# Kernel optimization log

Measured on AMD Instinct MI355X. Metric: run time of the kernel, lower is better.

Reference implementation:

```python
import jax, jax.numpy as jnp
import numpy as np

HIDDEN = 100
N_NODE = 100000
B = 512
T = 50

def setup_inputs() -> dict:
    key = jax.random.key(0)
    ks = jax.random.split(key, 20)
    stdv = 1.0 / np.sqrt(HIDDEN)
    u = lambda k, shape: jax.random.uniform(k, shape, jnp.float32, -stdv, stdv)
    d = HIDDEN
    return {
        "adj_in": jax.random.uniform(ks[0], (B, T, T), jnp.float32),
        "adj_out": jax.random.uniform(ks[1], (B, T, T), jnp.float32),
        "mask": jnp.ones((B, T), jnp.float32),
        "item": jax.random.randint(ks[2], (B, T), 0, N_NODE, jnp.int32),
        "alias": jax.random.randint(ks[3], (B, T), 0, T, jnp.int32),
        "step": 1,
        "embedding": u(ks[4], (N_NODE, d)),
        "W_in": u(ks[5], (d, d)),
        "b_in": u(ks[6], (d,)),
        "W_out": u(ks[7], (d, d)),
        "b_out": u(ks[8], (d,)),
        "gru_gate_k": u(ks[9], (3 * d, 2 * d)),
        "gru_gate_b": jnp.ones((2 * d,), jnp.float32),  # TF GRUCell gate bias init = 1.0
        "gru_cand_k": u(ks[10], (3 * d, d)),
        "gru_cand_b": jnp.zeros((d,), jnp.float32),
        "nasr_w1": u(ks[11], (d, d)),
        "nasr_w2": u(ks[12], (d, d)),
        "nasr_v": u(ks[13], (1, d)),
        "nasr_b": jnp.zeros((d,), jnp.float32),
        "B_mat": u(ks[14], (2 * d, d)),
    }


def _ggnn(item, adj_in, adj_out, embedding, W_in, b_in, W_out, b_out,
          gru_gate_k, gru_gate_b, gru_cand_k, gru_cand_b, step):
    h = embedding[item]  # [B,T,d]
    d = h.shape[-1]
    for _ in range(step):
        a_in = jnp.einsum('bts,bsd->btd', adj_in, h @ W_in + b_in)
        a_out = jnp.einsum('bts,bsd->btd', adj_out, h @ W_out + b_out)
        a = jnp.concatenate([a_in, a_out], axis=-1)  # [B,T,2d]
        # TF GRUCell: gates then candidate
        gates = jax.nn.sigmoid(jnp.concatenate([a, h], -1) @ gru_gate_k + gru_gate_b)
        r, u_ = gates[..., :d], gates[..., d:]
        c = jnp.tanh(jnp.concatenate([a, r * h], -1) @ gru_cand_k + gru_cand_b)
        h = u_ * h + (1.0 - u_) * c
    return h  # [B,T,d]


def reference(adj_in, adj_out, mask, item, alias, step, embedding,
              W_in, b_in, W_out, b_out, gru_gate_k, gru_gate_b,
              gru_cand_k, gru_cand_b, nasr_w1, nasr_w2, nasr_v, nasr_b, B_mat):
    d = embedding.shape[1]
    re_emb = _ggnn(item, adj_in, adj_out, embedding, W_in, b_in, W_out, b_out,
                   gru_gate_k, gru_gate_b, gru_cand_k, gru_cand_b, step)
    rm = jnp.sum(jax.lax.stop_gradient(mask), axis=1)  # session lengths
    bidx = jnp.arange(re_emb.shape[0])
    last_id = alias[bidx, rm.astype(jnp.int32) - 1]          # [B]
    last_h = re_emb[bidx, last_id]                            # [B,d]
    seq_h = jnp.take_along_axis(re_emb, alias[..., None], axis=1)  # [B,L,d]
    last = last_h @ nasr_w1                                   # [B,d]
    seq = seq_h @ nasr_w2                                     # [B,L,d]
    m = jax.nn.sigmoid(last[:, None, :] + seq + nasr_b)       # [B,L,d]
    coef = (m @ nasr_v[0]) * mask                             # [B,L]
    ma = jnp.concatenate([jnp.sum(coef[..., None] * seq_h, axis=1), last], axis=-1)  # [B,2d]
    y1 = ma @ B_mat                                           # [B,d]
    logits = y1 @ embedding[1:].T                             # [B,n_node-1]
    return logits
```

## Files before the change

### kernel.cpp

```cpp
#include <hip/hip_runtime.h>
#include <math.h>

#define D 100
#define T 50
#define BB 512
#define NOUT 99999

__device__ __forceinline__ float sigf(float x) { return 1.f / (1.f + expf(-x)); }

__global__ __launch_bounds__(256) void ggnn_fused(
    const float* __restrict__ adj_in, const float* __restrict__ adj_out,
    const float* __restrict__ mask,   const int* __restrict__ item,
    const int* __restrict__ alias_,   const float* __restrict__ emb,
    const float* __restrict__ W_in,   const float* __restrict__ b_in,
    const float* __restrict__ W_out,  const float* __restrict__ b_out,
    const float* __restrict__ gate_k, const float* __restrict__ gate_b,
    const float* __restrict__ cand_k, const float* __restrict__ cand_b,
    const float* __restrict__ w1,     const float* __restrict__ w2,
    const float* __restrict__ v,      const float* __restrict__ nb,
    const float* __restrict__ Bm,     float* __restrict__ y1)
{
    __shared__ float hS[T*D];
    __shared__ float R1[T*D];
    __shared__ float R2[T*D];
    __shared__ float maskS[T+2], vS[D], nbS[D], lastWS[D], coefS[T+2], maS[2*D];
    __shared__ int aliasS[T+2];
    __shared__ int rmidx;

    const int b = blockIdx.x, tid = threadIdx.x;
    const size_t bT = (size_t)b * T;

    if (tid < T) {
        aliasS[tid] = alias_[bT + tid];
        maskS[tid]  = mask[bT + tid];
    }
    if (tid >= 64 && tid < 64 + D) {
        int k = tid - 64;
        vS[k] = v[k]; nbS[k] = nb[k];
    }
    for (int idx = tid; idx < T*25; idx += 256) {
        int t = idx / 25, q = idx - t*25;
        int node = item[bT + t];
        *(float4*)&hS[t*D + q*4] = *(const float4*)&emb[(size_t)node*D + q*4];
    }
    __syncthreads();
    if (tid == 0) {
        float s = 0.f;
        for (int t = 0; t < T; ++t) s += maskS[t];
        rmidx = aliasS[(int)s - 1];
    }

    const bool act250 = tid < 250;
    const int tg50  = tid / 50;
    const int rem50 = tid % 50;
    const int cg25  = tid / 25;
    const int jq25  = tid % 25;

    if (act250) {
        const int which = rem50 / 25, jq = rem50 % 25;
        const int t0 = tg50 * 10;
        const float* W  = which ? W_out : W_in;
        const float* bb = which ? b_out : b_in;
        float4 binit = *(const float4*)&bb[jq*4];
        float4 acc[10];
        #pragma unroll
        for (int tt = 0; tt < 10; ++tt) acc[tt] = binit;
        for (int k = 0; k < D; k += 2) {
            float4 wa = *(const float4*)&W[k*D + jq*4];
            float4 wb = *(const float4*)&W[(k+1)*D + jq*4];
            #pragma unroll
            for (int tt = 0; tt < 10; ++tt) {
                float2 a = *(const float2*)&hS[(t0+tt)*D + k];
                acc[tt].x += a.x*wa.x + a.y*wb.x;
                acc[tt].y += a.x*wa.y + a.y*wb.y;
                acc[tt].z += a.x*wa.z + a.y*wb.z;
                acc[tt].w += a.x*wa.w + a.y*wb.w;
            }
        }
        float* dst = which ? R2 : R1;
        #pragma unroll
        for (int tt = 0; tt < 10; ++tt)
            *(float4*)&dst[(t0+tt)*D + jq*4] = acc[tt];
    }
    __syncthreads();

    float4 eacc[10];
    if (act250) {
        const int which = rem50 / 25, jq = rem50 % 25;
        const int t0 = tg50 * 10;
        const float* adj = which ? adj_out : adj_in;
        const float* Xs  = which ? R2 : R1;
        #pragma unroll
        for (int tt = 0; tt < 10; ++tt) eacc[tt] = make_float4(0.f,0.f,0.f,0.f);
        #pragma unroll 2
        for (int s = 0; s < T; ++s) {
            float4 x = *(const float4*)&Xs[s*D + jq*4];
            const float* ap = &adj[(bT + t0)*T + s];
            #pragma unroll
            for (int tt = 0; tt < 10; ++tt) {
                float a = ap[tt*T];
                eacc[tt].x += a*x.x; eacc[tt].y += a*x.y;
                eacc[tt].z += a*x.z; eacc[tt].w += a*x.w;
            }
        }
    }
    __syncthreads();
    if (act250) {
        const int which = rem50 / 25, jq = rem50 % 25;
        const int t0 = tg50 * 10;
        float* dst = which ? R2 : R1;
        #pragma unroll
        for (int tt = 0; tt < 10; ++tt)
            *(float4*)&dst[(t0+tt)*D + jq*4] = eacc[tt];
    }
    __syncthreads();

    float4 gacc[10];
    if (act250) {
        const int nq = rem50;
        const int t0 = tg50 * 10;
        float4 ginit = *(const float4*)&gate_b[nq*4];
        #pragma unroll
        for (int tt = 0; tt < 10; ++tt) gacc[tt] = ginit;
        for (int k = 0; k < D; k += 2) {
            float4 g0a = *(const float4*)&gate_k[(size_t)k*200 + nq*4];
            float4 g0b = *(const float4*)&gate_k[(size_t)(k+1)*200 + nq*4];
            float4 g1a = *(const float4*)&gate_k[(size_t)(k+100)*200 + nq*4];
            float4 g1b = *(const float4*)&gate_k[(size_t)(k+101)*200 + nq*4];
            float4 g2a = *(const float4*)&gate_k[(size_t)(k+200)*200 + nq*4];
            float4 g2b = *(const float4*)&gate_k[(size_t)(k+201)*200 + nq*4];
            #pragma unroll
            for (int tt = 0; tt < 10; ++tt) {
                float2 a0 = *(const float2*)&R1[(t0+tt)*D + k];
                float2 a1 = *(const float2*)&R2[(t0+tt)*D + k];
                float2 a2 = *(const float2*)&hS[(t0+tt)*D + k];
                gacc[tt].x += a0.x*g0a.x + a0.y*g0b.x + a1.x*g1a.x + a1.y*g1b.x + a2.x*g2a.x + a2.y*g2b.x;
                gacc[tt].y += a0.x*g0a.y + a0.y*g0b.y + a1.x*g1a.y + a1.y*g1b.y + a2.x*g2a.y + a2.y*g2b.y;
                gacc[tt].z += a0.x*g0a.z + a0.y*g0b.z + a1.x*g1a.z + a1.y*g1b.z + a2.x*g2a.z + a2.y*g2b.z;
                gacc[tt].w += a0.x*g0a.w + a0.y*g0b.w + a1.x*g1a.w + a1.y*g1b.w + a2.x*g2a.w + a2.y*g2b.w;
            }
        }
        #pragma unroll
        for (int tt = 0; tt < 10; ++tt) {
            gacc[tt].x = sigf(gacc[tt].x); gacc[tt].y = sigf(gacc[tt].y);
            gacc[tt].z = sigf(gacc[tt].z); gacc[tt].w = sigf(gacc[tt].w);
        }
    }

    float4 cacc[5];
    if (act250) {
        const int t0 = cg25 * 5;
        float4 cinit = *(const float4*)&cand_b[jq25*4];
        #pragma unroll
        for (int tt = 0; tt < 5; ++tt) cacc[tt] = cinit;
        for (int k = 0; k < D; k += 2) {
            float4 c0a = *(const float4*)&cand_k[(size_t)k*D + jq25*4];
            float4 c0b = *(const float4*)&cand_k[(size_t)(k+1)*D + jq25*4];
            float4 c1a = *(const float4*)&cand_k[(size_t)(k+100)*D + jq25*4];
            float4 c1b = *(const float4*)&cand_k[(size_t)(k+101)*D + jq25*4];
            #pragma unroll
            for (int tt = 0; tt < 5; ++tt) {
                float2 a0 = *(const float2*)&R1[(t0+tt)*D + k];
                float2 a1 = *(const float2*)&R2[(t0+tt)*D + k];
                cacc[tt].x += a0.x*c0a.x + a0.y*c0b.x + a1.x*c1a.x + a1.y*c1b.x;
                cacc[tt].y += a0.x*c0a.y + a0.y*c0b.y + a1.x*c1a.y + a1.y*c1b.y;
                cacc[tt].z += a0.x*c0a.z + a0.y*c0b.z + a1.x*c1a.z + a1.y*c1b.z;
                cacc[tt].w += a0.x*c0a.w + a0.y*c0b.w + a1.x*c1a.w + a1.y*c1b.w;
            }
        }
    }
    __syncthreads();

    if (act250) {
        const int nq = rem50;
        const int t0 = tg50 * 10;
        if (nq < 25) {
            #pragma unroll
            for (int tt = 0; tt < 10; ++tt) {
                float4 hh = *(const float4*)&hS[(t0+tt)*D + nq*4];
                float4 g = gacc[tt];
                float4 o; o.x = g.x*hh.x; o.y = g.y*hh.y; o.z = g.z*hh.z; o.w = g.w*hh.w;
                *(float4*)&R1[(t0+tt)*D + nq*4] = o;
            }
        } else {
            #pragma unroll
            for (int tt = 0; tt < 10; ++tt)
                *(float4*)&R2[(t0+tt)*D + (nq-25)*4] = gacc[tt];
        }
    }
    __syncthreads();

    if (act250) {
        const int t0 = cg25 * 5;
        for (int k = 0; k < D; k += 2) {
            float4 c2a = *(const float4*)&cand_k[(size_t)(k+200)*D + jq25*4];
            float4 c2b = *(const float4*)&cand_k[(size_t)(k+201)*D + jq25*4];
            #pragma unroll
            for (int tt = 0; tt < 5; ++tt) {
                float2 rh = *(const float2*)&R1[(t0+tt)*D + k];
                cacc[tt].x += rh.x*c2a.x + rh.y*c2b.x;
                cacc[tt].y += rh.x*c2a.y + rh.y*c2b.y;
                cacc[tt].z += rh.x*c2a.z + rh.y*c2b.z;
                cacc[tt].w += rh.x*c2a.w + rh.y*c2b.w;
            }
        }
        #pragma unroll
        for (int tt = 0; tt < 5; ++tt) {
            float4 c4;
            c4.x = tanhf(cacc[tt].x); c4.y = tanhf(cacc[tt].y);
            c4.z = tanhf(cacc[tt].z); c4.w = tanhf(cacc[tt].w);
            float4 u4 = *(const float4*)&R2[(t0+tt)*D + jq25*4];
            float4 hh = *(const float4*)&hS[(t0+tt)*D + jq25*4];
            float4 o;
            o.x = u4.x*hh.x + (1.f-u4.x)*c4.x;
            o.y = u4.y*hh.y + (1.f-u4.y)*c4.y;
            o.z = u4.z*hh.z + (1.f-u4.z)*c4.z;
            o.w = u4.w*hh.w + (1.f-u4.w)*c4.w;
            *(float4*)&hS[(t0+tt)*D + jq25*4] = o;
        }
    }
    __syncthreads();

    if (tid < 125) {
        const int sg = tid / 25, jq = tid % 25;
        const int t0 = sg * 10;
        float4 sacc[10];
        #pragma unroll
        for (int tt = 0; tt < 10; ++tt) sacc[tt] = make_float4(0.f,0.f,0.f,0.f);
        int at[10];
        #pragma unroll
        for (int tt = 0; tt < 10; ++tt) at[tt] = aliasS[t0+tt];
        for (int k = 0; k < D; k += 2) {
            float4 wa = *(const float4*)&w2[(size_t)k*D + jq*4];
            float4 wb = *(const float4*)&w2[(size_t)(k+1)*D + jq*4];
            #pragma unroll
            for (int tt = 0; tt < 10; ++tt) {
                float2 a = *(const float2*)&hS[at[tt]*D + k];
                sacc[tt].x += a.x*wa.x + a.y*wb.x;
                sacc[tt].y += a.x*wa.y + a.y*wb.y;
                sacc[tt].z += a.x*wa.z + a.y*wb.z;
                sacc[tt].w += a.x*wa.w + a.y*wb.w;
            }
        }
        #pragma unroll
        for (int tt = 0; tt < 10; ++tt)
            *(float4*)&R1[(t0+tt)*D + jq*4] = sacc[tt];
    } else if (tid >= 128 && tid < 153) {
        const int jq = tid - 128;
        const int lid = rmidx;
        float4 acc = make_float4(0.f,0.f,0.f,0.f);
        for (int k = 0; k < D; k += 2) {
            float4 wa = *(const float4*)&w1[(size_t)k*D + jq*4];
            float4 wb = *(const float4*)&w1[(size_t)(k+1)*D + jq*4];
            float2 a = *(const float2*)&hS[lid*D + k];
            acc.x += a.x*wa.x + a.y*wb.x;
            acc.y += a.x*wa.y + a.y*wb.y;
            acc.z += a.x*wa.z + a.y*wb.z;
            acc.w += a.x*wa.w + a.y*wb.w;
        }
        *(float4*)&lastWS[jq*4] = acc;
    }
    __syncthreads();

    if (tid < T) {
        float s = 0.f;
        #pragma unroll 4
        for (int k = 0; k < D; ++k) {
            float x = lastWS[k] + R1[tid*D + k] + nbS[k];
            s += vS[k] * sigf(x);
        }
        coefS[tid] = s * maskS[tid];
    }
    __syncthreads();
    if (tid < 25) {
        float4 acc = make_float4(0.f,0.f,0.f,0.f);
        #pragma unroll 5
        for (int t = 0; t < T; ++t) {
            float c = coefS[t];
            float4 hh = *(const float4*)&hS[aliasS[t]*D + tid*4];
            acc.x += c*hh.x; acc.y += c*hh.y; acc.z += c*hh.z; acc.w += c*hh.w;
        }
        *(float4*)&maS[tid*4] = acc;
    } else if (tid >= 32 && tid < 57) {
        int j4 = tid - 32;
        *(float4*)&maS[D + j4*4] = *(const float4*)&lastWS[j4*4];
    }
    __syncthreads();
    if (tid < 25) {
        float4 acc = make_float4(0.f,0.f,0.f,0.f);
        #pragma unroll 4
        for (int k = 0; k < 2*D; ++k) {
            float a = maS[k];
            float4 w = *(const float4*)&Bm[(size_t)k*D + tid*4];
            acc.x += a*w.x; acc.y += a*w.y; acc.z += a*w.z; acc.w += a*w.w;
        }
        *(float4*)&y1[(size_t)b*D + tid*4] = acc;
    }
}

#define LDB 132

#define GB_COMPUTE(Ab, kbase) do {                                            \
    _Pragma("unroll")                                                         \
    for (int kk = 0; kk < 4; ++kk) {                                          \
        float4 b0 = *(const float4*)&Bs[(kbase + kk)*LDB + tx*4];             \
        float4 b1 = *(const float4*)&Bs[(kbase + kk)*LDB + 64 + tx*4];        \
        _Pragma("unroll")                                                     \
        for (int i = 0; i < 8; ++i) {                                         \
            float a_ = kk==0 ? Ab[i].x : kk==1 ? Ab[i].y :                    \
                       kk==2 ? Ab[i].z : Ab[i].w;                             \
            acc[i][0] += a_*b0.x; acc[i][1] += a_*b0.y;                       \
            acc[i][2] += a_*b0.z; acc[i][3] += a_*b0.w;                       \
            acc[i][4] += a_*b1.x; acc[i][5] += a_*b1.y;                       \
            acc[i][6] += a_*b1.z; acc[i][7] += a_*b1.w;                       \
        }                                                                     \
    }                                                                         \
} while (0)

__global__ __launch_bounds__(256) void gemm_big(
    const float* __restrict__ y1,
    const float* __restrict__ emb,
    float* __restrict__ out)
{
    __shared__ float Bs[100*LDB];
    const int tid = threadIdx.x;
    const int tx = tid & 15, ty = tid >> 4;
    const int n0 = blockIdx.x * 128;

    for (int idx = tid; idx < 128*25; idx += 256) {
        int n = idx / 25, q = idx - n*25;
        int gn = n0 + n;
        float4 vv = make_float4(0.f,0.f,0.f,0.f);
        if (gn < NOUT) vv = *(const float4*)&emb[(size_t)(gn+1)*D + q*4];
        int w = n & 63;
        int pos = (n & 64) + ((w & 15) << 2) + (w >> 4);
        Bs[(q*4+0)*LDB + pos] = vv.x;
        Bs[(q*4+1)*LDB + pos] = vv.y;
        Bs[(q*4+2)*LDB + pos] = vv.z;
        Bs[(q*4+3)*LDB + pos] = vv.w;
    }
    __syncthreads();

    float acc[8][8];
    float4 A0[8], A1[8];

    #pragma unroll 1
    for (int mc = 0; mc < 2; ++mc) {
        const int m0 = blockIdx.y * 256 + mc * 128;

        #pragma unroll
        for (int i = 0; i < 8; ++i)
            #pragma unroll
            for (int j = 0; j < 8; ++j) acc[i][j] = 0.f;

        #pragma unroll
        for (int i = 0; i < 8; ++i)
            A0[i] = *(const float4*)&y1[(size_t)(m0 + ty + i*16)*D + 0];

        int k = 0;
        #pragma unroll 1
        for (int it = 0; it < 12; ++it, k += 8) {
            #pragma unroll
            for (int i = 0; i < 8; ++i)
                A1[i] = *(const float4*)&y1[(size_t)(m0 + ty + i*16)*D + k + 4];
            GB_COMPUTE(A0, k);
            #pragma unroll
            for (int i = 0; i < 8; ++i)
                A0[i] = *(const float4*)&y1[(size_t)(m0 + ty + i*16)*D + k + 8];
            GB_COMPUTE(A1, k + 4);
        }
        GB_COMPUTE(A0, 96);

        #pragma unroll
        for (int i = 0; i < 8; ++i) {
            size_t row = (size_t)(m0 + ty + i*16) * NOUT;
            #pragma unroll
            for (int h = 0; h < 2; ++h)
                #pragma unroll
                for (int q = 0; q < 4; ++q) {
                    int n = n0 + h*64 + q*16 + tx;
                    if (n < NOUT) out[row + n] = acc[i][h*4+q];
                }
        }
    }
}

extern "C" void kernel_launch(void* const* d_in, const int* in_sizes, int n_in,
                              void* d_out, int out_size, void* d_ws, size_t ws_size,
                              hipStream_t stream)
{
    const float* adj_in  = (const float*)d_in[0];
    const float* adj_out = (const float*)d_in[1];
    const float* mask    = (const float*)d_in[2];
    const int*   item    = (const int*)  d_in[3];
    const int*   alias_  = (const int*)  d_in[4];
    const float* emb     = (const float*)d_in[6];
    const float* W_in    = (const float*)d_in[7];
    const float* b_in    = (const float*)d_in[8];
    const float* W_out   = (const float*)d_in[9];
    const float* b_out   = (const float*)d_in[10];
    const float* gate_k  = (const float*)d_in[11];
    const float* gate_b  = (const float*)d_in[12];
    const float* cand_k  = (const float*)d_in[13];
    const float* cand_b  = (const float*)d_in[14];
    const float* w1      = (const float*)d_in[15];
    const float* w2      = (const float*)d_in[16];
    const float* v       = (const float*)d_in[17];
    const float* nb      = (const float*)d_in[18];
    const float* Bm      = (const float*)d_in[19];
    float* out = (float*)d_out;
    float* y1  = (float*)d_ws;

    ggnn_fused<<<BB, 256, 0, stream>>>(
        adj_in, adj_out, mask, item, alias_, emb,
        W_in, b_in, W_out, b_out, gate_k, gate_b, cand_k, cand_b,
        w1, w2, v, nb, Bm, y1);

    gemm_big<<<dim3((NOUT + 127)/128, 2), 256, 0, stream>>>(y1, emb, out);
}
```

Before: 635.5 us.

## Double GGNN block to 512 threads with split-K shuffle reductions

The fused GGNN kernel now launches 512 threads per block instead of 256. Each thread handles 5 timesteps instead of 10, and the candidate and w2 projections are split across thread pairs along K, then combined with __shfl_xor. This aims to raise parallelism and latency hiding in the per-session kernel and to cut per-thread register pressure. The cost is extra shuffles and more idle threads in the serial tail phases, and the big logits GEMM, which likely dominates the runtime, is unchanged.

After: 629.6 us. No clear change (-0.9%).

```diff
diff --git a/kernel.cpp b/kernel.cpp
--- a/kernel.cpp
+++ b/kernel.cpp
@@ -8,7 +8,7 @@
 
 __device__ __forceinline__ float sigf(float x) { return 1.f / (1.f + expf(-x)); }
 
-__global__ __launch_bounds__(256) void ggnn_fused(
+__global__ __launch_bounds__(512, 4) void ggnn_fused(
     const float* __restrict__ adj_in, const float* __restrict__ adj_out,
     const float* __restrict__ mask,   const int* __restrict__ item,
     const int* __restrict__ alias_,   const float* __restrict__ emb,
@@ -38,7 +38,7 @@
         int k = tid - 64;
         vS[k] = v[k]; nbS[k] = nb[k];
     }
-    for (int idx = tid; idx < T*25; idx += 256) {
+    for (int idx = tid; idx < T*25; idx += 512) {
         int t = idx / 25, q = idx - t*25;
         int node = item[bT + t];
         *(float4*)&hS[t*D + q*4] = *(const float4*)&emb[(size_t)node*D + q*4];
@@ -50,26 +50,22 @@
         rmidx = aliasS[(int)s - 1];
     }
 
-    const bool act250 = tid < 250;
-    const int tg50  = tid / 50;
-    const int rem50 = tid % 50;
-    const int cg25  = tid / 25;
-    const int jq25  = tid % 25;
-
-    if (act250) {
-        const int which = rem50 / 25, jq = rem50 % 25;
-        const int t0 = tg50 * 10;
+    const bool act500 = tid < 500;
+
+    if (act500) {
+        const int which = tid / 250, rem = tid % 250;
+        const int jq = rem % 25, t0 = (rem / 25) * 5;
         const float* W  = which ? W_out : W_in;
         const float* bb = which ? b_out : b_in;
         float4 binit = *(const float4*)&bb[jq*4];
-        float4 acc[10];
-        #pragma unroll
-        for (int tt = 0; tt < 10; ++tt) acc[tt] = binit;
+        float4 acc[5];
+        #pragma unroll
+        for (int tt = 0; tt < 5; ++tt) acc[tt] = binit;
         for (int k = 0; k < D; k += 2) {
             float4 wa = *(const float4*)&W[k*D + jq*4];
             float4 wb = *(const float4*)&W[(k+1)*D + jq*4];
             #pragma unroll
-            for (int tt = 0; tt < 10; ++tt) {
+            for (int tt = 0; tt < 5; ++tt) {
                 float2 a = *(const float2*)&hS[(t0+tt)*D + k];
                 acc[tt].x += a.x*wa.x + a.y*wb.x;
                 acc[tt].y += a.x*wa.y + a.y*wb.y;
@@ -79,25 +75,25 @@
         }
         float* dst = which ? R2 : R1;
         #pragma unroll
-        for (int tt = 0; tt < 10; ++tt)
+        for (int tt = 0; tt < 5; ++tt)
             *(float4*)&dst[(t0+tt)*D + jq*4] = acc[tt];
     }
     __syncthreads();
 
-    float4 eacc[10];
-    if (act250) {
-        const int which = rem50 / 25, jq = rem50 % 25;
-        const int t0 = tg50 * 10;
+    float4 eacc[5];
+    if (act500) {
+        const int which = tid / 250, rem = tid % 250;
+        const int jq = rem % 25, t0 = (rem / 25) * 5;
         const float* adj = which ? adj_out : adj_in;
         const float* Xs  = which ? R2 : R1;
         #pragma unroll
-        for (int tt = 0; tt < 10; ++tt) eacc[tt] = make_float4(0.f,0.f,0.f,0.f);
+        for (int tt = 0; tt < 5; ++tt) eacc[tt] = make_float4(0.f,0.f,0.f,0.f);
         #pragma unroll 2
         for (int s = 0; s < T; ++s) {
             float4 x = *(const float4*)&Xs[s*D + jq*4];
             const float* ap = &adj[(bT + t0)*T + s];
             #pragma unroll
-            for (int tt = 0; tt < 10; ++tt) {
+            for (int tt = 0; tt < 5; ++tt) {
                 float a = ap[tt*T];
                 eacc[tt].x += a*x.x; eacc[tt].y += a*x.y;
                 eacc[tt].z += a*x.z; eacc[tt].w += a*x.w;
@@ -105,23 +101,23 @@
         }
     }
     __syncthreads();
-    if (act250) {
-        const int which = rem50 / 25, jq = rem50 % 25;
-        const int t0 = tg50 * 10;
+    if (act500) {
+        const int which = tid / 250, rem = tid % 250;
+        const int jq = rem % 25, t0 = (rem / 25) * 5;
         float* dst = which ? R2 : R1;
         #pragma unroll
-        for (int tt = 0; tt < 10; ++tt)
+        for (int tt = 0; tt < 5; ++tt)
             *(float4*)&dst[(t0+tt)*D + jq*4] = eacc[tt];
     }
     __syncthreads();
 
-    float4 gacc[10];
-    if (act250) {
-        const int nq = rem50;
-        const int t0 = tg50 * 10;
+    float4 gacc[5];
+    if (act500) {
+        const int nq = tid % 50;
+        const int t0 = (tid / 50) * 5;
         float4 ginit = *(const float4*)&gate_b[nq*4];
         #pragma unroll
-        for (int tt = 0; tt < 10; ++tt) gacc[tt] = ginit;
+        for (int tt = 0; tt < 5; ++tt) gacc[tt] = ginit;
         for (int k = 0; k < D; k += 2) {
             float4 g0a = *(const float4*)&gate_k[(size_t)k*200 + nq*4];
             float4 g0b = *(const float4*)&gate_k[(size_t)(k+1)*200 + nq*4];
@@ -130,7 +126,7 @@
             float4 g2a = *(const float4*)&gate_k[(size_t)(k+200)*200 + nq*4];
             float4 g2b = *(const float4*)&gate_k[(size_t)(k+201)*200 + nq*4];
             #pragma unroll
-            for (int tt = 0; tt < 10; ++tt) {
+            for (int tt = 0; tt < 5; ++tt) {
                 float2 a0 = *(const float2*)&R1[(t0+tt)*D + k];
                 float2 a1 = *(const float2*)&R2[(t0+tt)*D + k];
                 float2 a2 = *(const float2*)&hS[(t0+tt)*D + k];
@@ -141,42 +137,44 @@
             }
         }
         #pragma unroll
-        for (int tt = 0; tt < 10; ++tt) {
+        for (int tt = 0; tt < 5; ++tt) {
             gacc[tt].x = sigf(gacc[tt].x); gacc[tt].y = sigf(gacc[tt].y);
             gacc[tt].z = sigf(gacc[tt].z); gacc[tt].w = sigf(gacc[tt].w);
         }
     }
 
     float4 cacc[5];
-    if (act250) {
-        const int t0 = cg25 * 5;
-        float4 cinit = *(const float4*)&cand_b[jq25*4];
+    if (act500) {
+        const int jq = (tid >> 1) % 25;
+        const int t0 = ((tid >> 1) / 25) * 5;
+        const int kh = tid & 1;
+        const float* Ck = cand_k + (size_t)(kh ? 100 : 0) * D;
+        const float* As = kh ? R2 : R1;
+        float4 bq = *(const float4*)&cand_b[jq*4];
+        float4 cinit = kh ? make_float4(0.f,0.f,0.f,0.f) : bq;
         #pragma unroll
         for (int tt = 0; tt < 5; ++tt) cacc[tt] = cinit;
-        for (int k = 0; k < D; k += 2) {
-            float4 c0a = *(const float4*)&cand_k[(size_t)k*D + jq25*4];
-            float4 c0b = *(const float4*)&cand_k[(size_t)(k+1)*D + jq25*4];
-            float4 c1a = *(const float4*)&cand_k[(size_t)(k+100)*D + jq25*4];
-            float4 c1b = *(const float4*)&cand_k[(size_t)(k+101)*D + jq25*4];
-            #pragma unroll
-            for (int tt = 0; tt < 5; ++tt) {
-                float2 a0 = *(const float2*)&R1[(t0+tt)*D + k];
-                float2 a1 = *(const float2*)&R2[(t0+tt)*D + k];
-                cacc[tt].x += a0.x*c0a.x + a0.y*c0b.x + a1.x*c1a.x + a1.y*c1b.x;
-                cacc[tt].y += a0.x*c0a.y + a0.y*c0b.y + a1.x*c1a.y + a1.y*c1b.y;
-                cacc[tt].z += a0.x*c0a.z + a0.y*c0b.z + a1.x*c1a.z + a1.y*c1b.z;
-                cacc[tt].w += a0.x*c0a.w + a0.y*c0b.w + a1.x*c1a.w + a1.y*c1b.w;
-            }
-        }
-    }
-    __syncthreads();
-
-    if (act250) {
-        const int nq = rem50;
-        const int t0 = tg50 * 10;
+        for (int k = 0; k < 100; k += 2) {
+            float4 ca = *(const float4*)&Ck[(size_t)k*D + jq*4];
+            float4 cb = *(const float4*)&Ck[(size_t)(k+1)*D + jq*4];
+            #pragma unroll
+            for (int tt = 0; tt < 5; ++tt) {
+                float2 a = *(const float2*)&As[(t0+tt)*D + k];
+                cacc[tt].x += a.x*ca.x + a.y*cb.x;
+                cacc[tt].y += a.x*ca.y + a.y*cb.y;
+                cacc[tt].z += a.x*ca.z + a.y*cb.z;
+                cacc[tt].w += a.x*ca.w + a.y*cb.w;
+            }
+        }
+    }
+    __syncthreads();
+
+    if (act500) {
+        const int nq = tid % 50;
+        const int t0 = (tid / 50) * 5;
         if (nq < 25) {
             #pragma unroll
-            for (int tt = 0; tt < 10; ++tt) {
+            for (int tt = 0; tt < 5; ++tt) {
                 float4 hh = *(const float4*)&hS[(t0+tt)*D + nq*4];
                 float4 g = gacc[tt];
                 float4 o; o.x = g.x*hh.x; o.y = g.y*hh.y; o.z = g.z*hh.z; o.w = g.w*hh.w;
@@ -184,58 +182,72 @@
             }
         } else {
             #pragma unroll
-            for (int tt = 0; tt < 10; ++tt)
+            for (int tt = 0; tt < 5; ++tt)
                 *(float4*)&R2[(t0+tt)*D + (nq-25)*4] = gacc[tt];
         }
     }
     __syncthreads();
 
-    if (act250) {
-        const int t0 = cg25 * 5;
-        for (int k = 0; k < D; k += 2) {
-            float4 c2a = *(const float4*)&cand_k[(size_t)(k+200)*D + jq25*4];
-            float4 c2b = *(const float4*)&cand_k[(size_t)(k+201)*D + jq25*4];
-            #pragma unroll
-            for (int tt = 0; tt < 5; ++tt) {
-                float2 rh = *(const float2*)&R1[(t0+tt)*D + k];
-                cacc[tt].x += rh.x*c2a.x + rh.y*c2b.x;
-                cacc[tt].y += rh.x*c2a.y + rh.y*c2b.y;
-                cacc[tt].z += rh.x*c2a.z + rh.y*c2b.z;
-                cacc[tt].w += rh.x*c2a.w + rh.y*c2b.w;
+    if (act500) {
+        const int jq = (tid >> 1) % 25;
+        const int t0 = ((tid >> 1) / 25) * 5;
+        const int kh = tid & 1;
+        const float* Ck3 = cand_k + (size_t)(200 + kh*50) * D;
+        for (int k = 0; k < 50; k += 2) {
+            float4 ca = *(const float4*)&Ck3[(size_t)k*D + jq*4];
+            float4 cb = *(const float4*)&Ck3[(size_t)(k+1)*D + jq*4];
+            #pragma unroll
+            for (int tt = 0; tt < 5; ++tt) {
+                float2 rh = *(const float2*)&R1[(t0+tt)*D + kh*50 + k];
+                cacc[tt].x += rh.x*ca.x + rh.y*cb.x;
+                cacc[tt].y += rh.x*ca.y + rh.y*cb.y;
+                cacc[tt].z += rh.x*ca.z + rh.y*cb.z;
+                cacc[tt].w += rh.x*ca.w + rh.y*cb.w;
             }
         }
         #pragma unroll
         for (int tt = 0; tt < 5; ++tt) {
-            float4 c4;
-            c4.x = tanhf(cacc[tt].x); c4.y = tanhf(cacc[tt].y);
-            c4.z = tanhf(cacc[tt].z); c4.w = tanhf(cacc[tt].w);
-            float4 u4 = *(const float4*)&R2[(t0+tt)*D + jq25*4];
-            float4 hh = *(const float4*)&hS[(t0+tt)*D + jq25*4];
-            float4 o;
-            o.x = u4.x*hh.x + (1.f-u4.x)*c4.x;
-            o.y = u4.y*hh.y + (1.f-u4.y)*c4.y;
-            o.z = u4.z*hh.z + (1.f-u4.z)*c4.z;
-            o.w = u4.w*hh.w + (1.f-u4.w)*c4.w;
-            *(float4*)&hS[(t0+tt)*D + jq25*4] = o;
-        }
-    }
-    __syncthreads();
-
-    if (tid < 125) {
-        const int sg = tid / 25, jq = tid % 25;
-        const int t0 = sg * 10;
-        float4 sacc[10];
-        #pragma unroll
-        for (int tt = 0; tt < 10; ++tt) sacc[tt] = make_float4(0.f,0.f,0.f,0.f);
-        int at[10];
-        #pragma unroll
-        for (int tt = 0; tt < 10; ++tt) at[tt] = aliasS[t0+tt];
-        for (int k = 0; k < D; k += 2) {
-            float4 wa = *(const float4*)&w2[(size_t)k*D + jq*4];
-            float4 wb = *(const float4*)&w2[(size_t)(k+1)*D + jq*4];
-            #pragma unroll
-            for (int tt = 0; tt < 10; ++tt) {
-                float2 a = *(const float2*)&hS[at[tt]*D + k];
+            cacc[tt].x += __shfl_xor(cacc[tt].x, 1);
+            cacc[tt].y += __shfl_xor(cacc[tt].y, 1);
+            cacc[tt].z += __shfl_xor(cacc[tt].z, 1);
+            cacc[tt].w += __shfl_xor(cacc[tt].w, 1);
+        }
+        if (!kh) {
+            #pragma unroll
+            for (int tt = 0; tt < 5; ++tt) {
+                float4 c4;
+                c4.x = tanhf(cacc[tt].x); c4.y = tanhf(cacc[tt].y);
+                c4.z = tanhf(cacc[tt].z); c4.w = tanhf(cacc[tt].w);
+                float4 u4 = *(const float4*)&R2[(t0+tt)*D + jq*4];
+                float4 hh = *(const float4*)&hS[(t0+tt)*D + jq*4];
+                float4 o;
+                o.x = u4.x*hh.x + (1.f-u4.x)*c4.x;
+                o.y = u4.y*hh.y + (1.f-u4.y)*c4.y;
+                o.z = u4.z*hh.z + (1.f-u4.z)*c4.z;
+                o.w = u4.w*hh.w + (1.f-u4.w)*c4.w;
+                *(float4*)&hS[(t0+tt)*D + jq*4] = o;
+            }
+        }
+    }
+    __syncthreads();
+
+    if (act500) {
+        const int jq = (tid >> 1) % 25;
+        const int t0 = ((tid >> 1) / 25) * 5;
+        const int kh = tid & 1;
+        float4 sacc[5];
+        #pragma unroll
+        for (int tt = 0; tt < 5; ++tt) sacc[tt] = make_float4(0.f,0.f,0.f,0.f);
+        int at[5];
+        #pragma unroll
+        for (int tt = 0; tt < 5; ++tt) at[tt] = aliasS[t0+tt];
+        const float* Wp = w2 + (size_t)(kh*50) * D;
+        for (int k = 0; k < 50; k += 2) {
+            float4 wa = *(const float4*)&Wp[(size_t)k*D + jq*4];
+            float4 wb = *(const float4*)&Wp[(size_t)(k+1)*D + jq*4];
+            #pragma unroll
+            for (int tt = 0; tt < 5; ++tt) {
+                float2 a = *(const float2*)&hS[at[tt]*D + kh*50 + k];
                 sacc[tt].x += a.x*wa.x + a.y*wb.x;
                 sacc[tt].y += a.x*wa.y + a.y*wb.y;
                 sacc[tt].z += a.x*wa.z + a.y*wb.z;
@@ -243,22 +255,33 @@
             }
         }
         #pragma unroll
-        for (int tt = 0; tt < 10; ++tt)
-            *(float4*)&R1[(t0+tt)*D + jq*4] = sacc[tt];
-    } else if (tid >= 128 && tid < 153) {
-        const int jq = tid - 128;
+        for (int tt = 0; tt < 5; ++tt) {
+            sacc[tt].x += __shfl_xor(sacc[tt].x, 1);
+            sacc[tt].y += __shfl_xor(sacc[tt].y, 1);
+            sacc[tt].z += __shfl_xor(sacc[tt].z, 1);
+            sacc[tt].w += __shfl_xor(sacc[tt].w, 1);
+        }
+        if (!kh) {
+            #pragma unroll
+            for (int tt = 0; tt < 5; ++tt)
+                *(float4*)&R1[(t0+tt)*D + jq*4] = sacc[tt];
+        }
+    } else {
+        const int u = tid - 500;
         const int lid = rmidx;
-        float4 acc = make_float4(0.f,0.f,0.f,0.f);
-        for (int k = 0; k < D; k += 2) {
-            float4 wa = *(const float4*)&w1[(size_t)k*D + jq*4];
-            float4 wb = *(const float4*)&w1[(size_t)(k+1)*D + jq*4];
-            float2 a = *(const float2*)&hS[lid*D + k];
-            acc.x += a.x*wa.x + a.y*wb.x;
-            acc.y += a.x*wa.y + a.y*wb.y;
-            acc.z += a.x*wa.z + a.y*wb.z;
-            acc.w += a.x*wa.w + a.y*wb.w;
-        }
-        *(float4*)&lastWS[jq*4] = acc;
+        for (int jq = u; jq < 25; jq += 12) {
+            float4 acc = make_float4(0.f,0.f,0.f,0.f);
+            for (int k = 0; k < D; k += 2) {
+                float4 wa = *(const float4*)&w1[(size_t)k*D + jq*4];
+                float4 wb = *(const float4*)&w1[(size_t)(k+1)*D + jq*4];
+                float2 a = *(const float2*)&hS[lid*D + k];
+                acc.x += a.x*wa.x + a.y*wb.x;
+                acc.y += a.x*wa.y + a.y*wb.y;
+                acc.z += a.x*wa.z + a.y*wb.z;
+                acc.w += a.x*wa.w + a.y*wb.w;
+            }
+            *(float4*)&lastWS[jq*4] = acc;
+        }
     }
     __syncthreads();
 
@@ -411,7 +434,7 @@
     float* out = (float*)d_out;
     float* y1  = (float*)d_ws;
 
-    ggnn_fused<<<BB, 256, 0, stream>>>(
+    ggnn_fused<<<BB, 512, 0, stream>>>(
         adj_in, adj_out, mask, item, alias_, emb,
         W_in, b_in, W_out, b_out, gate_k, gate_b, cand_k, cand_b,
         w1, w2, v, nb, Bm, y1);
```
